# Performance work log

Hardware: AMD Instinct MI355X
Metric: run time of the kernel (lower is better)

The kernel has to match this reference:

```python
import jax, jax.numpy as jnp
import numpy as np

B, S, H = 1, 1024, 2048
E, F, FS = 32, 768, 4096
TOP_K = 4
SCALE = 0.02


def setup_inputs() -> dict:
    key = jax.random.key(0)
    ks = jax.random.split(key, 9)
    return {
        "hidden_states": jax.random.normal(ks[0], (B, S, H), jnp.float32),
        "router_weight": jax.random.normal(ks[1], (E, H), jnp.float32) * SCALE,
        "w_gate": jax.random.normal(ks[2], (E, H, F), jnp.float32) * SCALE,
        "w_up": jax.random.normal(ks[3], (E, H, F), jnp.float32) * SCALE,
        "w_down": jax.random.normal(ks[4], (E, F, H), jnp.float32) * SCALE,
        "sw_gate": jax.random.normal(ks[5], (H, FS), jnp.float32) * SCALE,
        "sw_up": jax.random.normal(ks[6], (H, FS), jnp.float32) * SCALE,
        "sw_down": jax.random.normal(ks[7], (FS, H), jnp.float32) * SCALE,
        "sgate_w": jax.random.normal(ks[8], (H, 1), jnp.float32) * SCALE,
    }


def reference(hidden_states, router_weight, w_gate, w_up, w_down,
              sw_gate, sw_up, sw_down, sgate_w):
    b, s, h = hidden_states.shape
    x = hidden_states.reshape(-1, h)                      # [T,H]
    T = x.shape[0]

    # ---- router: linear -> softmax (fp32) -> topk -> renormalize ----
    logits = x @ router_weight.T                          # [T,E]
    probs = jax.nn.softmax(logits.astype(jnp.float32), axis=-1)
    topv, topi = jax.lax.top_k(probs, TOP_K)              # [T,K]
    topv = topv / jnp.sum(topv, axis=-1, keepdims=True)
    topv = topv.astype(probs.dtype)

    # combine weights: scatter topk weights into dense [T,E] mask
    combine = jnp.zeros((T, E), probs.dtype).at[
        jnp.arange(T)[:, None], topi].add(topv)

    # ---- experts: SwiGLU per expert, weighted combine ----
    g = jnp.einsum('th,ehf->etf', x, w_gate)              # [E,T,F]
    u = jnp.einsum('th,ehf->etf', x, w_up)                # [E,T,F]
    act = jax.nn.silu(g) * u                              # [E,T,F]
    out = jnp.einsum('te,etf,efh->th', combine, act, w_down)  # [T,H]

    # ---- shared expert with sigmoid gate ----
    shared = (jax.nn.silu(x @ sw_gate) * (x @ sw_up)) @ sw_down  # [T,H]
    out = out + jax.nn.sigmoid(x @ sgate_w) * shared

    return out.reshape(b, s, h)
```

## Files before the change

kernel.cpp:

```cpp
#include <hip/hip_runtime.h>
#include <math.h>

#define T_TOK 1024
#define H_DIM 2048
#define N_EXP 32
#define TOPK  4
#define F_DIM 768
#define FS_DIM 4096
#define FS_HALF 2048

typedef __bf16 bf16;
typedef __attribute__((ext_vector_type(4))) __bf16 bf16x4;
typedef __attribute__((ext_vector_type(8))) __bf16 bf16x8;
typedef __attribute__((ext_vector_type(4))) float f32x4;

#define BAR() do {                                        \
    asm volatile("s_waitcnt lgkmcnt(0)" ::: "memory");    \
    __builtin_amdgcn_s_barrier();                         \
    __builtin_amdgcn_sched_barrier(0);                    \
  } while (0)

__device__ __forceinline__ int swz(int row, int colB) {
  return row * 64 + (colB ^ (((row >> 2) & 3) << 4));
}

__global__ __launch_bounds__(256) void router_kernel(
    const float* __restrict__ x, const float* __restrict__ rw,
    const float* __restrict__ sgw,
    float* __restrict__ topw, float* __restrict__ sg,
    int* __restrict__ counts, int* __restrict__ lists)
{
  int t = blockIdx.x; int tid = threadIdx.x;
  int lane = tid & 63, wave = tid >> 6;
  float acc[N_EXP];
  #pragma unroll
  for (int e = 0; e < N_EXP; e++) acc[e] = 0.f;
  float accs = 0.f;
  const float* xr = x + (size_t)t * H_DIM;
  for (int h = tid; h < H_DIM; h += 256) {
    float xv = xr[h];
    accs += xv * sgw[h];
    #pragma unroll
    for (int e = 0; e < N_EXP; e++) acc[e] += xv * rw[e * H_DIM + h];
  }
  __shared__ float red[4][N_EXP];
  __shared__ float reds[4];
  __shared__ float logits[N_EXP];
  #pragma unroll
  for (int e = 0; e < N_EXP; e++) {
    float v = acc[e];
    for (int off = 32; off; off >>= 1) v += __shfl_down(v, off, 64);
    if (lane == 0) red[wave][e] = v;
  }
  {
    float v = accs;
    for (int off = 32; off; off >>= 1) v += __shfl_down(v, off, 64);
    if (lane == 0) reds[wave] = v;
  }
  __syncthreads();
  if (tid < N_EXP) logits[tid] = red[0][tid] + red[1][tid] + red[2][tid] + red[3][tid];
  __syncthreads();
  if (tid == 0) {
    float m = -1e30f;
    #pragma unroll
    for (int e = 0; e < N_EXP; e++) m = fmaxf(m, logits[e]);
    float p[N_EXP];
    #pragma unroll
    for (int e = 0; e < N_EXP; e++) p[e] = expf(logits[e] - m);
    int ids[TOPK]; float vs[TOPK]; float wsum = 0.f;
    #pragma unroll
    for (int k = 0; k < TOPK; k++) {
      int best = 0; float bv = -1.f;
      for (int e = 0; e < N_EXP; e++) {
        if (p[e] > bv) { bv = p[e]; best = e; }
      }
      ids[k] = best; vs[k] = bv; wsum += bv; p[best] = -2.f;
    }
    float inv = 1.f / wsum;
    float sgs = reds[0] + reds[1] + reds[2] + reds[3];
    sg[t] = 1.f / (1.f + expf(-sgs));
    #pragma unroll
    for (int k = 0; k < TOPK; k++) {
      int slot = t * TOPK + k;
      topw[slot] = vs[k] * inv;
      int pos = atomicAdd(&counts[ids[k]], 1);
      lists[ids[k] * T_TOK + pos] = slot;
    }
  }
}

__global__ __launch_bounds__(512, 4) void gateup_fused(
    const float* __restrict__ X,
    const float* __restrict__ wg_, const float* __restrict__ wu_,
    const float* __restrict__ swg, const float* __restrict__ swu,
    bf16* __restrict__ act, bf16* __restrict__ acts,
    const int* __restrict__ lists, const int* __restrict__ counts,
    int n_shared, int sh_nfb, int actsN, int col_off)
{
  int id = blockIdx.x;
  bool gather = id >= n_shared;
  const float *Wg, *Wu; const int* lb = nullptr;
  int count, mt, fb, ldb, Nout; bf16* C;
  if (gather) {
    int g = id - n_shared;
    int j = g >> 3;
    int e = (g & 7) + 8 * (j / 96);
    int rr = j % 96;
    mt = (rr / 6) * 64; fb = (rr % 6) * 128;
    count = counts[e]; lb = lists + e * T_TOK;
    Wg = wg_ + (size_t)e * H_DIM * F_DIM;
    Wu = wu_ + (size_t)e * H_DIM * F_DIM;
    ldb = F_DIM; Nout = F_DIM; C = act;
  } else {
    fb = (id % sh_nfb) * 128; mt = (id / sh_nfb) * 64;
    count = T_TOK; ldb = FS_DIM; Nout = actsN;
    Wg = swg + col_off; Wu = swu + col_off;
    C = acts;
  }
  if (mt >= count) return;

  __shared__ alignas(16) char sA [2][64 * 64];
  __shared__ alignas(16) char sBg[2][128 * 64];
  __shared__ alignas(16) char sBu[2][128 * 64];

  int tid = threadIdx.x;
  int lane = tid & 63, wid = tid >> 6;
  int wr = wid >> 2, wc = wid & 3;
  int l15 = lane & 15, qB = (lane >> 4) << 4;

  const float* aptr;
  {
    int r = mt + (tid >> 3);
    int rc = r < count ? r : count - 1;
    int tok = gather ? (lb[rc] >> 2) : rc;
    aptr = X + (size_t)tok * H_DIM + ((tid & 7) << 2);
  }
  int t8 = tid & 255;
  int bng = t8 & 31;
  int bk4 = (t8 >> 5) << 2;
  const float* bptr = (tid < 256 ? Wg : Wu) + (size_t)bk4 * ldb + fb + bng * 4;
  char* bds = (tid < 256) ? &sBg[0][0] : &sBu[0][0];

  f32x4 accg[2][2], accu[2][2];
  #pragma unroll
  for (int m = 0; m < 2; m++)
    #pragma unroll
    for (int n = 0; n < 2; n++) {
      accg[m][n] = (f32x4){0.f,0.f,0.f,0.f};
      accu[m][n] = (f32x4){0.f,0.f,0.f,0.f};
    }

  f32x4 ava, bva[4];
  f32x4 avb, bvb[4];

  #define GU_ISSUE(av, bv, k0) do {                                   \
    av = *(const f32x4*)(aptr + (k0));                                \
    _Pragma("unroll")                                                 \
    for (int r_ = 0; r_ < 4; r_++)                                    \
      bv[r_] = *(const f32x4*)(bptr + (size_t)((k0) + r_) * ldb);     \
  } while (0)

  #define GU_STAGE(b, av, bv) do {                                    \
    bf16x4 ta;                                                        \
    ta[0]=(bf16)av[0]; ta[1]=(bf16)av[1];                             \
    ta[2]=(bf16)av[2]; ta[3]=(bf16)av[3];                             \
    *(bf16x4*)(sA[b] + swz(tid >> 3, (tid & 7) << 3)) = ta;           \
    _Pragma("unroll")                                                 \
    for (int i_ = 0; i_ < 4; i_++) {                                  \
      bf16x4 tb;                                                      \
      tb[0]=(bf16)bv[0][i_]; tb[1]=(bf16)bv[1][i_];                   \
      tb[2]=(bf16)bv[2][i_]; tb[3]=(bf16)bv[3][i_];                   \
      *(bf16x4*)(bds + (b) * (128 * 64) + swz(bng * 4 + i_, bk4 << 1)) = tb; \
    } } while (0)

  #define GU_MFMA(b) do {                                             \
    __builtin_amdgcn_s_setprio(1);                                    \
    bf16x8 af0 = *(const bf16x8*)(sA[b] + swz(wr * 32 + l15, qB));    \
    bf16x8 af1 = *(const bf16x8*)(sA[b] + swz(wr * 32 + 16 + l15, qB)); \
    _Pragma("unroll")                                                 \
    for (int n_ = 0; n_ < 2; n_++) {                                  \
      int rb = wc * 32 + n_ * 16 + l15;                               \
      bf16x8 bg = *(const bf16x8*)(sBg[b] + swz(rb, qB));             \
      bf16x8 bu = *(const bf16x8*)(sBu[b] + swz(rb, qB));             \
      accg[0][n_] = __builtin_amdgcn_mfma_f32_16x16x32_bf16(af0, bg, accg[0][n_], 0,0,0); \
      accg[1][n_] = __builtin_amdgcn_mfma_f32_16x16x32_bf16(af1, bg, accg[1][n_], 0,0,0); \
      accu[0][n_] = __builtin_amdgcn_mfma_f32_16x16x32_bf16(af0, bu, accu[0][n_], 0,0,0); \
      accu[1][n_] = __builtin_amdgcn_mfma_f32_16x16x32_bf16(af1, bu, accu[1][n_], 0,0,0); \
    }                                                                 \
    __builtin_amdgcn_s_setprio(0);                                    \
  } while (0)

  const int NT = H_DIM / 32;
  GU_ISSUE(ava, bva, 0);
  GU_ISSUE(avb, bvb, 32);
  GU_STAGE(0, ava, bva);
  GU_ISSUE(ava, bva, 64);
  BAR();
  for (int t = 0; t < NT; t += 2) {
    GU_MFMA(0);
    GU_STAGE(1, avb, bvb);
    if (t + 3 < NT) GU_ISSUE(avb, bvb, (t + 3) * 32);
    BAR();
    GU_MFMA(1);
    if (t + 2 < NT) {
      GU_STAGE(0, ava, bva);
      if (t + 4 < NT) GU_ISSUE(ava, bva, (t + 4) * 32);
    }
    BAR();
  }
  #undef GU_ISSUE
  #undef GU_STAGE
  #undef GU_MFMA

  #pragma unroll
  for (int m = 0; m < 2; m++) {
    #pragma unroll
    for (int q = 0; q < 4; q++) {
      int gr = mt + wr * 32 + m * 16 + (lane >> 4) * 4 + q;
      if (gr < count) {
        size_t rowo = (gather ? (size_t)lb[gr] : (size_t)gr) * Nout;
        #pragma unroll
        for (int n = 0; n < 2; n++) {
          float g = accg[m][n][q], u = accu[m][n][q];
          C[rowo + fb + wc * 32 + n * 16 + l15] =
              (bf16)(g / (1.f + __expf(-g)) * u);
        }
      }
    }
  }
}

__global__ __launch_bounds__(256, 4) void down_fused(
    const bf16* __restrict__ act, const bf16* __restrict__ acts,
    const float* __restrict__ wd_, const float* __restrict__ swd,
    bf16* __restrict__ dslot, float* __restrict__ out,
    const float* __restrict__ sg,
    const int* __restrict__ lists, const int* __restrict__ counts,
    int n_shared, int lda_sh, int kd_sh, int swd_off, int accum)
{
  int id = blockIdx.x;
  bool expert = id >= n_shared;
  const bf16* A; const float* W; const int* lb = nullptr;
  int count, mt, nb, Kd, lda;
  if (expert) {
    int g = id - n_shared;
    int j = g >> 3;
    int e = (g & 7) + 8 * (j >> 7);
    int rr = j & 127;
    nb = (rr & 15) * 128; mt = (rr >> 4) * 64;
    count = counts[e]; lb = lists + e * T_TOK;
    A = act; lda = F_DIM; Kd = F_DIM;
    W = wd_ + (size_t)e * F_DIM * H_DIM;
  } else {
    nb = (id & 15) * 128; mt = (id >> 4) * 64;
    count = T_TOK; A = acts; lda = lda_sh; Kd = kd_sh;
    W = swd + (size_t)swd_off * H_DIM;
  }
  if (mt >= count) return;

  __shared__ alignas(16) char sA[2][64 * 64];
  __shared__ alignas(16) char sB[2][128 * 64];

  int tid = threadIdx.x;
  int lane = tid & 63, wid = tid >> 6;
  int wr = wid >> 1, wc = wid & 1;
  int l15 = lane & 15, qB = (lane >> 4) << 4;
  int bng = tid & 31;
  int bk4 = (tid >> 5) << 2;

  const bf16* aptr;
  {
    int r = mt + (tid >> 2);
    int rc = r < count ? r : count - 1;
    int ar = expert ? lb[rc] : rc;
    aptr = A + (size_t)ar * lda + ((tid & 3) << 3);
  }
  const float* bptr = W + (size_t)bk4 * H_DIM + nb + bng * 4;

  f32x4 acc[2][4];
  #pragma unroll
  for (int m = 0; m < 2; m++)
    #pragma unroll
    for (int n = 0; n < 4; n++)
      acc[m][n] = (f32x4){0.f,0.f,0.f,0.f};

  uint4 ava, avb; f32x4 bva[4], bvb[4];

  #define DN_ISSUE(av, bv, k0) do {                                   \
    av = *(const uint4*)(aptr + (k0));                                \
    _Pragma("unroll")                                                 \
    for (int r_ = 0; r_ < 4; r_++)                                    \
      bv[r_] = *(const f32x4*)(bptr + (size_t)((k0) + r_) * H_DIM);   \
    } while (0)

  #define DN_STAGE(b, av, bv) do {                                    \
    *(uint4*)(sA[b] + swz(tid >> 2, (tid & 3) << 4)) = av;            \
    _Pragma("unroll")                                                 \
    for (int i_ = 0; i_ < 4; i_++) {                                  \
      bf16x4 tb;                                                      \
      tb[0]=(bf16)bv[0][i_]; tb[1]=(bf16)bv[1][i_];                   \
      tb[2]=(bf16)bv[2][i_]; tb[3]=(bf16)bv[3][i_];                   \
      *(bf16x4*)(sB[b] + swz(bng * 4 + i_, bk4 << 1)) = tb;           \
    } } while (0)

  #define DN_MFMA(b) do {                                             \
    __builtin_amdgcn_s_setprio(1);                                    \
    bf16x8 af0 = *(const bf16x8*)(sA[b] + swz(wr * 32 + l15, qB));    \
    bf16x8 af1 = *(const bf16x8*)(sA[b] + swz(wr * 32 + 16 + l15, qB)); \
    _Pragma("unroll")                                                 \
    for (int n_ = 0; n_ < 4; n_++) {                                  \
      bf16x8 bb = *(const bf16x8*)(sB[b] + swz(wc * 64 + n_ * 16 + l15, qB)); \
      acc[0][n_] = __builtin_amdgcn_mfma_f32_16x16x32_bf16(af0, bb, acc[0][n_], 0,0,0); \
      acc[1][n_] = __builtin_amdgcn_mfma_f32_16x16x32_bf16(af1, bb, acc[1][n_], 0,0,0); \
    }                                                                 \
    __builtin_amdgcn_s_setprio(0);                                    \
  } while (0)

  const int NT = Kd / 32;
  DN_ISSUE(ava, bva, 0);
  DN_ISSUE(avb, bvb, 32);
  DN_STAGE(0, ava, bva);
  DN_ISSUE(ava, bva, 64);
  BAR();
  for (int t = 0; t < NT; t += 2) {
    DN_MFMA(0);
    DN_STAGE(1, avb, bvb);
    if (t + 3 < NT) DN_ISSUE(avb, bvb, (t + 3) * 32);
    BAR();
    DN_MFMA(1);
    if (t + 2 < NT) {
      DN_STAGE(0, ava, bva);
      if (t + 4 < NT) DN_ISSUE(ava, bva, (t + 4) * 32);
    }
    BAR();
  }
  #undef DN_ISSUE
  #undef DN_STAGE
  #undef DN_MFMA

  #pragma unroll
  for (int m = 0; m < 2; m++) {
    #pragma unroll
    for (int q = 0; q < 4; q++) {
      int gr = mt + wr * 32 + m * 16 + (lane >> 4) * 4 + q;
      if (gr < count) {
        #pragma unroll
        for (int n = 0; n < 4; n++) {
          int col = nb + wc * 64 + n * 16 + l15;
          if (expert) {
            dslot[(size_t)lb[gr] * H_DIM + col] = (bf16)acc[m][n][q];
          } else if (!accum) {
            out[(size_t)gr * H_DIM + col] = sg[gr] * acc[m][n][q];
          } else {
            out[(size_t)gr * H_DIM + col] += sg[gr] * acc[m][n][q];
          }
        }
      }
    }
  }
}

__global__ __launch_bounds__(256) void combine_kernel(
    const bf16* __restrict__ dslot, const float* __restrict__ topw,
    float* __restrict__ out)
{
  int t = blockIdx.x;
  int h = threadIdx.x * 8;
  float w0 = topw[t * 4 + 0], w1 = topw[t * 4 + 1];
  float w2 = topw[t * 4 + 2], w3 = topw[t * 4 + 3];
  bf16x8 a0 = *(const bf16x8*)&dslot[(size_t)(t * 4 + 0) * H_DIM + h];
  bf16x8 a1 = *(const bf16x8*)&dslot[(size_t)(t * 4 + 1) * H_DIM + h];
  bf16x8 a2 = *(const bf16x8*)&dslot[(size_t)(t * 4 + 2) * H_DIM + h];
  bf16x8 a3 = *(const bf16x8*)&dslot[(size_t)(t * 4 + 3) * H_DIM + h];
  f32x4 o0 = *(f32x4*)&out[(size_t)t * H_DIM + h];
  f32x4 o1 = *(f32x4*)&out[(size_t)t * H_DIM + h + 4];
  float o[8] = {o0[0], o0[1], o0[2], o0[3], o1[0], o1[1], o1[2], o1[3]};
  #pragma unroll
  for (int j = 0; j < 8; j++)
    o[j] += w0 * (float)a0[j] + w1 * (float)a1[j] + w2 * (float)a2[j]
          + w3 * (float)a3[j];
  *(f32x4*)&out[(size_t)t * H_DIM + h]     = (f32x4){o[0], o[1], o[2], o[3]};
  *(f32x4*)&out[(size_t)t * H_DIM + h + 4] = (f32x4){o[4], o[5], o[6], o[7]};
}

extern "C" void kernel_launch(void* const* d_in, const int* in_sizes, int n_in,
                              void* d_out, int out_size, void* d_ws, size_t ws_size,
                              hipStream_t stream) {
  const float* x   = (const float*)d_in[0];
  const float* rw  = (const float*)d_in[1];
  const float* wg  = (const float*)d_in[2];
  const float* wu  = (const float*)d_in[3];
  const float* wd  = (const float*)d_in[4];
  const float* swg = (const float*)d_in[5];
  const float* swu = (const float*)d_in[6];
  const float* swd = (const float*)d_in[7];
  const float* sgw = (const float*)d_in[8];
  float* out = (float*)d_out;
  char* ws = (char*)d_ws;

  bool fullfs = ws_size >= (size_t)32000000;
  size_t actsN = fullfs ? FS_DIM : FS_HALF;
  int sh_nfb = (int)(actsN / 128);
  int nsh_gu = sh_nfb * (T_TOK / 64);

  size_t off = 0;
  int*   counts  = (int*)(ws + off); off += 256;
  int*   lists   = (int*)(ws + off); off += (size_t)N_EXP * T_TOK * 4;
  float* topw    = (float*)(ws + off); off += (size_t)T_TOK * TOPK * 4;
  float* sg      = (float*)(ws + off); off += (size_t)T_TOK * 4;
  bf16*  act     = (bf16*)(ws + off); off += (size_t)T_TOK * TOPK * F_DIM * 2;
  bf16*  acts    = (bf16*)(ws + off); off += (size_t)T_TOK * actsN * 2;
  bf16*  dslot   = (bf16*)(ws + off); off += (size_t)T_TOK * TOPK * H_DIM * 2;

  hipMemsetAsync(counts, 0, 256, stream);

  router_kernel<<<T_TOK, 256, 0, stream>>>(x, rw, sgw, topw, sg, counts, lists);

  const int EXP_GU = N_EXP * 96;
  const int DN_EXP = N_EXP * 128;

  if (fullfs) {
    gateup_fused<<<nsh_gu + EXP_GU, 512, 0, stream>>>(
        x, wg, wu, swg, swu, act, acts, lists, counts,
        nsh_gu, sh_nfb, FS_DIM, 0);
    down_fused<<<256 + DN_EXP, 256, 0, stream>>>(
        act, acts, wd, swd, dslot, out, sg, lists, counts,
        256, FS_DIM, FS_DIM, 0, 0);
  } else {
    gateup_fused<<<nsh_gu + EXP_GU, 512, 0, stream>>>(
        x, wg, wu, swg, swu, act, acts, lists, counts,
        nsh_gu, sh_nfb, FS_HALF, 0);
    down_fused<<<256 + DN_EXP, 256, 0, stream>>>(
        act, acts, wd, swd, dslot, out, sg, lists, counts,
        256, FS_HALF, FS_HALF, 0, 0);
    gateup_fused<<<nsh_gu, 512, 0, stream>>>(
        x, wg, wu, swg, swu, act, acts, lists, counts,
        nsh_gu, sh_nfb, FS_HALF, FS_HALF);
    down_fused<<<256, 256, 0, stream>>>(
        act, acts, wd, swd, dslot, out, sg, lists, counts,
        256, FS_HALF, FS_HALF, FS_HALF, 1);
  }
  combine_kernel<<<T_TOK, 256, 0, stream>>>(dslot, topw, out);
}
```

Before: 375.7 us.

## Split fused gate/up GEMM into two passes storing gate in bf16

Replaces the single 512-thread gate+up kernel with two 256-thread launches. The first computes the gate projection and writes it as bf16 into the activation buffer. The second computes the up projection, reads the stored gate, and applies SiLU·up in its epilogue. The aim is to cut LDS and register use per block (launch bounds go to 256 threads, 3 blocks). The cost is an extra launch, re-reading X, a round trip of the gate values through memory, and rounding the gate to bf16 before SiLU.

```diff
diff --git a/kernel.cpp b/kernel.cpp
--- a/kernel.cpp
+++ b/kernel.cpp
@@ -89,128 +89,120 @@
   }
 }
 
-__global__ __launch_bounds__(512, 4) void gateup_fused(
+template<int UMODE>
+__global__ __launch_bounds__(256, 3) void gu_pass(
     const float* __restrict__ X,
-    const float* __restrict__ wg_, const float* __restrict__ wu_,
-    const float* __restrict__ swg, const float* __restrict__ swu,
+    const float* __restrict__ wmat, const float* __restrict__ smat,
     bf16* __restrict__ act, bf16* __restrict__ acts,
     const int* __restrict__ lists, const int* __restrict__ counts,
     int n_shared, int sh_nfb, int actsN, int col_off)
 {
   int id = blockIdx.x;
   bool gather = id >= n_shared;
-  const float *Wg, *Wu; const int* lb = nullptr;
+  const float* W; const int* lb = nullptr;
   int count, mt, fb, ldb, Nout; bf16* C;
   if (gather) {
     int g = id - n_shared;
     int j = g >> 3;
-    int e = (g & 7) + 8 * (j / 96);
-    int rr = j % 96;
+    int e = (g & 7) + 8 * (j / 48);
+    int rr = j % 48;
     mt = (rr / 6) * 64; fb = (rr % 6) * 128;
     count = counts[e]; lb = lists + e * T_TOK;
-    Wg = wg_ + (size_t)e * H_DIM * F_DIM;
-    Wu = wu_ + (size_t)e * H_DIM * F_DIM;
+    W = wmat + (size_t)e * H_DIM * F_DIM;
     ldb = F_DIM; Nout = F_DIM; C = act;
   } else {
     fb = (id % sh_nfb) * 128; mt = (id / sh_nfb) * 64;
     count = T_TOK; ldb = FS_DIM; Nout = actsN;
-    Wg = swg + col_off; Wu = swu + col_off;
+    W = smat + col_off;
     C = acts;
   }
   if (mt >= count) return;
 
-  __shared__ alignas(16) char sA [2][64 * 64];
-  __shared__ alignas(16) char sBg[2][128 * 64];
-  __shared__ alignas(16) char sBu[2][128 * 64];
+  __shared__ alignas(16) char sA[2][64 * 64];
+  __shared__ alignas(16) char sB[2][128 * 64];
 
   int tid = threadIdx.x;
   int lane = tid & 63, wid = tid >> 6;
-  int wr = wid >> 2, wc = wid & 3;
+  int wr = wid >> 1, wc = wid & 1;
   int l15 = lane & 15, qB = (lane >> 4) << 4;
+  int bng = tid & 31;
+  int bk4 = (tid >> 5) << 2;
 
   const float* aptr;
   {
-    int r = mt + (tid >> 3);
+    int r = mt + (tid >> 2);
     int rc = r < count ? r : count - 1;
     int tok = gather ? (lb[rc] >> 2) : rc;
-    aptr = X + (size_t)tok * H_DIM + ((tid & 7) << 2);
-  }
-  int t8 = tid & 255;
-  int bng = t8 & 31;
-  int bk4 = (t8 >> 5) << 2;
-  const float* bptr = (tid < 256 ? Wg : Wu) + (size_t)bk4 * ldb + fb + bng * 4;
-  char* bds = (tid < 256) ? &sBg[0][0] : &sBu[0][0];
-
-  f32x4 accg[2][2], accu[2][2];
+    aptr = X + (size_t)tok * H_DIM + ((tid & 3) << 3);
+  }
+  const float* bptr = W + (size_t)bk4 * ldb + fb + bng * 4;
+
+  f32x4 acc[2][4];
   #pragma unroll
   for (int m = 0; m < 2; m++)
     #pragma unroll
-    for (int n = 0; n < 2; n++) {
-      accg[m][n] = (f32x4){0.f,0.f,0.f,0.f};
-      accu[m][n] = (f32x4){0.f,0.f,0.f,0.f};
-    }
-
-  f32x4 ava, bva[4];
-  f32x4 avb, bvb[4];
-
-  #define GU_ISSUE(av, bv, k0) do {                                   \
-    av = *(const f32x4*)(aptr + (k0));                                \
+    for (int n = 0; n < 4; n++)
+      acc[m][n] = (f32x4){0.f,0.f,0.f,0.f};
+
+  f32x4 av0a, av1a, av0b, av1b; f32x4 bva[4], bvb[4];
+
+  #define GP_ISSUE(a0, a1, bv, k0) do {                               \
+    a0 = *(const f32x4*)(aptr + (k0));                                \
+    a1 = *(const f32x4*)(aptr + (k0) + 4);                            \
     _Pragma("unroll")                                                 \
     for (int r_ = 0; r_ < 4; r_++)                                    \
       bv[r_] = *(const f32x4*)(bptr + (size_t)((k0) + r_) * ldb);     \
-  } while (0)
-
-  #define GU_STAGE(b, av, bv) do {                                    \
-    bf16x4 ta;                                                        \
-    ta[0]=(bf16)av[0]; ta[1]=(bf16)av[1];                             \
-    ta[2]=(bf16)av[2]; ta[3]=(bf16)av[3];                             \
-    *(bf16x4*)(sA[b] + swz(tid >> 3, (tid & 7) << 3)) = ta;           \
+    } while (0)
+
+  #define GP_STAGE(b, a0, a1, bv) do {                                \
+    bf16x8 t8;                                                        \
+    _Pragma("unroll")                                                 \
+    for (int j_ = 0; j_ < 4; j_++) {                                  \
+      t8[j_] = (bf16)a0[j_]; t8[4 + j_] = (bf16)a1[j_];               \
+    }                                                                 \
+    *(bf16x8*)(sA[b] + swz(tid >> 2, (tid & 3) << 4)) = t8;           \
     _Pragma("unroll")                                                 \
     for (int i_ = 0; i_ < 4; i_++) {                                  \
       bf16x4 tb;                                                      \
       tb[0]=(bf16)bv[0][i_]; tb[1]=(bf16)bv[1][i_];                   \
       tb[2]=(bf16)bv[2][i_]; tb[3]=(bf16)bv[3][i_];                   \
-      *(bf16x4*)(bds + (b) * (128 * 64) + swz(bng * 4 + i_, bk4 << 1)) = tb; \
+      *(bf16x4*)(sB[b] + swz(bng * 4 + i_, bk4 << 1)) = tb;           \
     } } while (0)
 
-  #define GU_MFMA(b) do {                                             \
+  #define GP_MFMA(b) do {                                             \
     __builtin_amdgcn_s_setprio(1);                                    \
     bf16x8 af0 = *(const bf16x8*)(sA[b] + swz(wr * 32 + l15, qB));    \
     bf16x8 af1 = *(const bf16x8*)(sA[b] + swz(wr * 32 + 16 + l15, qB)); \
     _Pragma("unroll")                                                 \
-    for (int n_ = 0; n_ < 2; n_++) {                                  \
-      int rb = wc * 32 + n_ * 16 + l15;                               \
-      bf16x8 bg = *(const bf16x8*)(sBg[b] + swz(rb, qB));             \
-      bf16x8 bu = *(const bf16x8*)(sBu[b] + swz(rb, qB));             \
-      accg[0][n_] = __builtin_amdgcn_mfma_f32_16x16x32_bf16(af0, bg, accg[0][n_], 0,0,0); \
-      accg[1][n_] = __builtin_amdgcn_mfma_f32_16x16x32_bf16(af1, bg, accg[1][n_], 0,0,0); \
-      accu[0][n_] = __builtin_amdgcn_mfma_f32_16x16x32_bf16(af0, bu, accu[0][n_], 0,0,0); \
-      accu[1][n_] = __builtin_amdgcn_mfma_f32_16x16x32_bf16(af1, bu, accu[1][n_], 0,0,0); \
+    for (int n_ = 0; n_ < 4; n_++) {                                  \
+      bf16x8 bb = *(const bf16x8*)(sB[b] + swz(wc * 64 + n_ * 16 + l15, qB)); \
+      acc[0][n_] = __builtin_amdgcn_mfma_f32_16x16x32_bf16(af0, bb, acc[0][n_], 0,0,0); \
+      acc[1][n_] = __builtin_amdgcn_mfma_f32_16x16x32_bf16(af1, bb, acc[1][n_], 0,0,0); \
     }                                                                 \
     __builtin_amdgcn_s_setprio(0);                                    \
   } while (0)
 
   const int NT = H_DIM / 32;
-  GU_ISSUE(ava, bva, 0);
-  GU_ISSUE(avb, bvb, 32);
-  GU_STAGE(0, ava, bva);
-  GU_ISSUE(ava, bva, 64);
+  GP_ISSUE(av0a, av1a, bva, 0);
+  GP_ISSUE(av0b, av1b, bvb, 32);
+  GP_STAGE(0, av0a, av1a, bva);
+  GP_ISSUE(av0a, av1a, bva, 64);
   BAR();
   for (int t = 0; t < NT; t += 2) {
-    GU_MFMA(0);
-    GU_STAGE(1, avb, bvb);
-    if (t + 3 < NT) GU_ISSUE(avb, bvb, (t + 3) * 32);
+    GP_MFMA(0);
+    GP_STAGE(1, av0b, av1b, bvb);
+    if (t + 3 < NT) GP_ISSUE(av0b, av1b, bvb, (t + 3) * 32);
     BAR();
-    GU_MFMA(1);
+    GP_MFMA(1);
     if (t + 2 < NT) {
-      GU_STAGE(0, ava, bva);
-      if (t + 4 < NT) GU_ISSUE(ava, bva, (t + 4) * 32);
+      GP_STAGE(0, av0a, av1a, bva);
+      if (t + 4 < NT) GP_ISSUE(av0a, av1a, bva, (t + 4) * 32);
     }
     BAR();
   }
-  #undef GU_ISSUE
-  #undef GU_STAGE
-  #undef GU_MFMA
+  #undef GP_ISSUE
+  #undef GP_STAGE
+  #undef GP_MFMA
 
   #pragma unroll
   for (int m = 0; m < 2; m++) {
@@ -220,10 +212,15 @@
       if (gr < count) {
         size_t rowo = (gather ? (size_t)lb[gr] : (size_t)gr) * Nout;
         #pragma unroll
-        for (int n = 0; n < 2; n++) {
-          float g = accg[m][n][q], u = accu[m][n][q];
-          C[rowo + fb + wc * 32 + n * 16 + l15] =
-              (bf16)(g / (1.f + __expf(-g)) * u);
+        for (int n = 0; n < 4; n++) {
+          int col = fb + wc * 64 + n * 16 + l15;
+          if (UMODE == 0) {
+            C[rowo + col] = (bf16)acc[m][n][q];
+          } else {
+            float g = (float)C[rowo + col];
+            float u = acc[m][n][q];
+            C[rowo + col] = (bf16)(g / (1.f + __expf(-g)) * u);
+          }
         }
       }
     }
@@ -416,26 +413,29 @@
 
   router_kernel<<<T_TOK, 256, 0, stream>>>(x, rw, sgw, topw, sg, counts, lists);
 
-  const int EXP_GU = N_EXP * 96;
+  const int EXP_GU = N_EXP * 48;
   const int DN_EXP = N_EXP * 128;
 
   if (fullfs) {
-    gateup_fused<<<nsh_gu + EXP_GU, 512, 0, stream>>>(
-        x, wg, wu, swg, swu, act, acts, lists, counts,
-        nsh_gu, sh_nfb, FS_DIM, 0);
+    gu_pass<0><<<nsh_gu + EXP_GU, 256, 0, stream>>>(
+        x, wg, swg, act, acts, lists, counts, nsh_gu, sh_nfb, FS_DIM, 0);
+    gu_pass<1><<<nsh_gu + EXP_GU, 256, 0, stream>>>(
+        x, wu, swu, act, acts, lists, counts, nsh_gu, sh_nfb, FS_DIM, 0);
     down_fused<<<256 + DN_EXP, 256, 0, stream>>>(
         act, acts, wd, swd, dslot, out, sg, lists, counts,
         256, FS_DIM, FS_DIM, 0, 0);
   } else {
-    gateup_fused<<<nsh_gu + EXP_GU, 512, 0, stream>>>(
-        x, wg, wu, swg, swu, act, acts, lists, counts,
-        nsh_gu, sh_nfb, FS_HALF, 0);
+    gu_pass<0><<<nsh_gu + EXP_GU, 256, 0, stream>>>(
+        x, wg, swg, act, acts, lists, counts, nsh_gu, sh_nfb, FS_HALF, 0);
+    gu_pass<1><<<nsh_gu + EXP_GU, 256, 0, stream>>>(
+        x, wu, swu, act, acts, lists, counts, nsh_gu, sh_nfb, FS_HALF, 0);
     down_fused<<<256 + DN_EXP, 256, 0, stream>>>(
         act, acts, wd, swd, dslot, out, sg, lists, counts,
         256, FS_HALF, FS_HALF, 0, 0);
-    gateup_fused<<<nsh_gu, 512, 0, stream>>>(
-        x, wg, wu, swg, swu, act, acts, lists, counts,
-        nsh_gu, sh_nfb, FS_HALF, FS_HALF);
+    gu_pass<0><<<nsh_gu, 256, 0, stream>>>(
+        x, wg, swg, act, acts, lists, counts, nsh_gu, sh_nfb, FS_HALF, FS_HALF);
+    gu_pass<1><<<nsh_gu, 256, 0, stream>>>(
+        x, wu, swu, act, acts, lists, counts, nsh_gu, sh_nfb, FS_HALF, FS_HALF);
     down_fused<<<256, 256, 0, stream>>>(
         act, acts, wd, swd, dslot, out, sg, lists, counts,
         256, FS_HALF, FS_HALF, FS_HALF, 1);
```

Measured after the change: 409.8 us. +9.1%, slower.
